# Performance work log

Measured on AMD Instinct MI355X. Metric: run time of the kernel, lower is better.

## Reference

```python
import jax, jax.numpy as jnp
import numpy as np

C_IN = 256
C_OUT = 256
NUM_HEADS = 4
C_HEAD = C_OUT // NUM_HEADS  # 64
ALPHA = 0.2
NEG_FILL = -9e15


def setup_inputs() -> dict:
    key = jax.random.key(0)
    k1, k2, k3, k4, k5 = jax.random.split(key, 5)
    B, N = 1, 4096
    node_feats = jax.random.normal(k1, (B, N, C_IN), dtype=jnp.float32)
    adj_matrix = jax.random.randint(k2, (B, N, N), 0, 2, dtype=jnp.int32)
    # xavier_uniform with gain=1.414 on projection weight (fan_in=C_IN, fan_out=C_OUT)
    lim_w = 1.414 * np.sqrt(6.0 / (C_IN + C_OUT))
    W = jax.random.uniform(k3, (C_IN, C_OUT), dtype=jnp.float32, minval=-lim_w, maxval=lim_w)
    b = jnp.zeros((C_OUT,), dtype=jnp.float32)
    lim_a = 1.414 * np.sqrt(6.0 / (NUM_HEADS + 2 * C_HEAD))
    a = jax.random.uniform(k4, (NUM_HEADS, 2 * C_HEAD), dtype=jnp.float32, minval=-lim_a, maxval=lim_a)
    return {"node_feats": node_feats, "adj_matrix": adj_matrix, "W": W, "b": b, "a": a}


def reference(node_feats, adj_matrix, W, b, a):
    B, N, _ = node_feats.shape
    # linear projection -> (B, N, H, C_HEAD)
    feats = (node_feats @ W + b).reshape(B, N, NUM_HEADS, C_HEAD)
    # attention logit for edge (i -> j): a_src . h_i + a_dst . h_j, per head
    a_src, a_dst = a[:, :C_HEAD], a[:, C_HEAD:]
    src = jnp.einsum('bnhc,hc->bnh', feats, a_src)  # indexed by row i
    dst = jnp.einsum('bnhc,hc->bnh', feats, a_dst)  # indexed by col j
    logits = src[:, :, None, :] + dst[:, None, :, :]  # (B, N, N, H)
    logits = jnp.where(logits >= 0, logits, ALPHA * logits)  # LeakyReLU(0.2)
    attn = jnp.where(adj_matrix[..., None] == 1, logits, NEG_FILL)
    probs = jax.nn.softmax(attn, axis=2)  # softmax over source nodes j
    out = jnp.einsum('bijh,bjhc->bihc', probs, feats)
    return out.reshape(B, N, NUM_HEADS * C_HEAD)  # concat heads
```

## Files before the change

kernel.cpp:

```cpp
#include <hip/hip_runtime.h>

#define NN 4096
#define C 256
#define NH 4
#define CH 64
#define JSPLIT 16
#define JSLICE (NN / JSPLIT)
#define NJT (JSLICE / 32)

typedef float f32x4 __attribute__((ext_vector_type(4)));
typedef __bf16 b16x8 __attribute__((ext_vector_type(8)));
typedef unsigned short u16x8 __attribute__((ext_vector_type(8)));
typedef unsigned int u32x4 __attribute__((ext_vector_type(4)));

__device__ inline float fast_exp2(float x) {
#if __has_builtin(__builtin_amdgcn_exp2f)
  return __builtin_amdgcn_exp2f(x);
#else
  return exp2f(x);
#endif
}

__device__ inline unsigned pack2bf(float f0, float f1) {
  unsigned u0 = __float_as_uint(f0) + 0x8000u;
  unsigned u1 = __float_as_uint(f1) + 0x8000u;
  return __builtin_amdgcn_perm(u1, u0, 0x07060302u);
}

__global__ __launch_bounds__(256) void k_prep(
    const int* __restrict__ adj, const float* __restrict__ X,
    const float* __restrict__ W, unsigned char* __restrict__ packed,
    unsigned short* __restrict__ Xbf, unsigned short* __restrict__ WT) {
  const int b = blockIdx.x, t = threadIdx.x;
  if (b < 8192) {
    const int idx = b * 256 + t;
    const int4 a0 = *(const int4*)(adj + (size_t)idx * 8);
    const int4 a1 = *(const int4*)(adj + (size_t)idx * 8 + 4);
    unsigned m = 0;
    m |= (a0.x != 0) ? 1u : 0u;   m |= (a0.y != 0) ? 2u : 0u;
    m |= (a0.z != 0) ? 4u : 0u;   m |= (a0.w != 0) ? 8u : 0u;
    m |= (a1.x != 0) ? 16u : 0u;  m |= (a1.y != 0) ? 32u : 0u;
    m |= (a1.z != 0) ? 64u : 0u;  m |= (a1.w != 0) ? 128u : 0u;
    packed[idx] = (unsigned char)m;
  } else if (b < 9216) {
    const int idx = (b - 8192) * 256 + t;
    const float4 v = ((const float4*)X)[idx];
    uint2 st;
    st.x = pack2bf(v.x, v.y);
    st.y = pack2bf(v.z, v.w);
    ((uint2*)Xbf)[idx] = st;
  } else {
    const int c = b - 9216;
    const float w = W[(size_t)t * C + c];
    WT[(size_t)c * C + t] = (unsigned short)((__float_as_uint(w) + 0x8000u) >> 16);
  }
}

__global__ __launch_bounds__(256) void k_feats(
    const unsigned short* __restrict__ Xbf, const unsigned short* __restrict__ WT,
    const float* __restrict__ bias, const float* __restrict__ av,
    unsigned short* __restrict__ F, float2* __restrict__ srcAB,
    float2* __restrict__ EdT2) {
  const int i0 = blockIdx.x * 16;
  const int h = threadIdx.x >> 6;
  const int lane = threadIdx.x & 63;
  const int q = lane >> 4, n = lane & 15;
  const int c0 = h * CH;
  const float LOG2E = 1.4426950408889634f;

  const f32x4 zero = {0.f, 0.f, 0.f, 0.f};
  f32x4 acc[4];
#pragma unroll
  for (int g = 0; g < 4; ++g) acc[g] = zero;

  const unsigned short* ap = Xbf + (size_t)(i0 + n) * C + q * 8;
#pragma unroll
  for (int kt = 0; kt < 8; ++kt) {
    const b16x8 aF = __builtin_bit_cast(b16x8, *(const u16x8*)(ap + kt * 32));
#pragma unroll
    for (int g = 0; g < 4; ++g) {
      const b16x8 bF = __builtin_bit_cast(b16x8,
          *(const u16x8*)(WT + (size_t)(c0 + g * 16 + n) * C + kt * 32 + q * 8));
      acc[g] = __builtin_amdgcn_mfma_f32_16x16x32_bf16(aF, bF, acc[g], 0, 0, 0);
    }
  }

  float fb[4][4], asv[4], adv[4];
#pragma unroll
  for (int g = 0; g < 4; ++g) {
    const float bs = bias[c0 + g * 16 + n];
    asv[g] = av[h * 128 + g * 16 + n];
    adv[g] = av[h * 128 + 64 + g * 16 + n];
#pragma unroll
    for (int r = 0; r < 4; ++r) fb[g][r] = acc[g][r] + bs;
  }
  const int jt = i0 >> 5, half = (i0 >> 4) & 1;
  const int qp = half * 2 + (q >> 1);
#pragma unroll
  for (int g = 0; g < 4; ++g) {
    uint2 st;
    st.x = pack2bf(fb[g][0], fb[g][1]);
    st.y = pack2bf(fb[g][2], fb[g][3]);
    *(uint2*)(F + ((size_t)((jt * NH + h) * 4 + g)) * 512 + (qp * 16 + n) * 8 + 4 * (q & 1)) = st;
  }
#pragma unroll
  for (int r = 0; r < 4; ++r) {
    float p = 0.f, d = 0.f;
#pragma unroll
    for (int g = 0; g < 4; ++g) {
      p = fmaf(fb[g][r], asv[g], p);
      d = fmaf(fb[g][r], adv[g], d);
    }
#pragma unroll
    for (int m = 1; m < 16; m <<= 1) {
      p += __shfl_xor(p, m);
      d += __shfl_xor(d, m);
    }
    if (n == 0) {
      const int row = i0 + q * 4 + r;
      const float dL = d * LOG2E;
      EdT2[(size_t)h * NN + row] = make_float2(fast_exp2(dL), fast_exp2(0.2f * dL));
      const float x = p + 16.0f;
      const float m2 = fmaxf(x, 0.2f * x) * LOG2E;
      srcAB[(size_t)row * NH + h] = make_float2(
          fast_exp2(fmaf(p, LOG2E, -m2)),
          fast_exp2(fmaf(0.2f * p, LOG2E, -m2)));
    }
  }
}

__global__ __launch_bounds__(256, 4) void k_attn(
    const unsigned char* __restrict__ packed,
    const unsigned short* __restrict__ F,
    const float2* __restrict__ srcAB, const float2* __restrict__ EdT2,
    _Float16* __restrict__ pacc, float* __restrict__ lpart) {
  const int slice = blockIdx.x;
  const int i0 = blockIdx.y * 32;
  const int h = threadIdx.x >> 6;
  const int lane = threadIdx.x & 63;
  const int q = lane >> 4, n = lane & 15;
  const int jbase = slice * JSLICE;

  const int r0 = i0 + n, r1 = i0 + 16 + n;
  const float2 ab0 = srcAB[(size_t)r0 * NH + h];
  const float2 ab1 = srcAB[(size_t)r1 * NH + h];

  const f32x4 zero = {0.f, 0.f, 0.f, 0.f};
  f32x4 acc0[4], acc1[4], lacc0 = zero, lacc1 = zero;
#pragma unroll
  for (int g = 0; g < 4; ++g) { acc0[g] = zero; acc1[g] = zero; }

  u16x8 ou;
#pragma unroll
  for (int jj = 0; jj < 8; ++jj) ou[jj] = 0x3F80;
  const b16x8 ones = __builtin_bit_cast(b16x8, ou);

  const uint2 m20 = *(const uint2*)(packed + (size_t)r0 * 512 + (jbase >> 3) + q * 8);
  const uint2 m21 = *(const uint2*)(packed + (size_t)r1 * 512 + (jbase >> 3) + q * 8);

  const float* dp2 = (const float*)(EdT2 + (size_t)h * NN + jbase);
  const unsigned short* fp = F + ((size_t)((jbase >> 5) * NH + h) * 4) * 512 + lane * 8;

#pragma unroll
  for (int a = 0; a < 4; ++a) {
#pragma unroll
    for (int b = 0; b < 2; ++b) {
      const int jt = a * 2 + b;
      b16x8 bF[4];
#pragma unroll
      for (int g = 0; g < 4; ++g)
        bF[g] = __builtin_bit_cast(b16x8,
            *(const u16x8*)(fp + (size_t)(jt * NH * 4 + g) * 512));

      const int w0 = b ? (int)m20.y : (int)m20.x;
      const int w1 = b ? (int)m21.y : (int)m21.x;
      const unsigned Mb0 = (unsigned(__shfl(w0, a * 16 + n)) >> (q * 8)) & 0xffu;
      const unsigned Mb1 = (unsigned(__shfl(w1, a * 16 + n)) >> (q * 8)) & 0xffu;

      const float* dq = dp2 + jt * 64 + q * 16;
      const float4 dd0 = *(const float4*)(dq);
      const float4 dd1 = *(const float4*)(dq + 4);
      const float4 dd2 = *(const float4*)(dq + 8);
      const float4 dd3 = *(const float4*)(dq + 12);
      const float4 dd[4] = {dd0, dd1, dd2, dd3};

      u32x4 pk0, pk1;
#pragma unroll
      for (int k = 0; k < 4; ++k) {
        const float4 d = dd[k];
        const float e00 = (Mb0 & (1u << (2 * k))) ? fmaxf(d.x * ab0.x, d.y * ab0.y) : 0.f;
        const float e01 = (Mb0 & (2u << (2 * k))) ? fmaxf(d.z * ab0.x, d.w * ab0.y) : 0.f;
        const float e10 = (Mb1 & (1u << (2 * k))) ? fmaxf(d.x * ab1.x, d.y * ab1.y) : 0.f;
        const float e11 = (Mb1 & (2u << (2 * k))) ? fmaxf(d.z * ab1.x, d.w * ab1.y) : 0.f;
        pk0[k] = pack2bf(e00, e01);
        pk1[k] = pack2bf(e10, e11);
      }
      const b16x8 E0 = __builtin_bit_cast(b16x8, pk0);
      const b16x8 E1 = __builtin_bit_cast(b16x8, pk1);
#pragma unroll
      for (int g = 0; g < 4; ++g) {
        acc0[g] = __builtin_amdgcn_mfma_f32_16x16x32_bf16(E0, bF[g], acc0[g], 0, 0, 0);
        acc1[g] = __builtin_amdgcn_mfma_f32_16x16x32_bf16(E1, bF[g], acc1[g], 0, 0, 0);
      }
      lacc0 = __builtin_amdgcn_mfma_f32_16x16x32_bf16(E0, ones, lacc0, 0, 0, 0);
      lacc1 = __builtin_amdgcn_mfma_f32_16x16x32_bf16(E1, ones, lacc1, 0, 0, 0);
    }
  }

#pragma unroll
  for (int g = 0; g < 4; ++g)
#pragma unroll
    for (int r = 0; r < 4; ++r) {
      const int col = h * CH + g * 16 + n;
      pacc[((size_t)slice * NN + i0 + q * 4 + r) * C + col] = (_Float16)acc0[g][r];
      pacc[((size_t)slice * NN + i0 + 16 + q * 4 + r) * C + col] = (_Float16)acc1[g][r];
    }
  if (n == 0) {
#pragma unroll
    for (int r = 0; r < 4; ++r) {
      lpart[((size_t)slice * NN + i0 + q * 4 + r) * NH + h] = lacc0[r];
      lpart[((size_t)slice * NN + i0 + 16 + q * 4 + r) * NH + h] = lacc1[r];
    }
  }
}

__global__ __launch_bounds__(256) void k_final(
    const _Float16* __restrict__ pacc, const float* __restrict__ lpart,
    float* __restrict__ out) {
  const int i = blockIdx.x;
  const int c = threadIdx.x;
  const int h = c >> 6;
  float l = 0.f, sa = 0.f;
#pragma unroll
  for (int sp = 0; sp < JSPLIT; ++sp) {
    l += lpart[((size_t)sp * NN + i) * NH + h];
    sa += (float)pacc[((size_t)sp * NN + i) * C + c];
  }
  out[(size_t)i * C + c] = sa / l;
}

extern "C" void kernel_launch(void* const* d_in, const int* in_sizes, int n_in,
                              void* d_out, int out_size, void* d_ws, size_t ws_size,
                              hipStream_t stream) {
  const float* nf   = (const float*)d_in[0];
  const int* adj    = (const int*)d_in[1];
  const float* W    = (const float*)d_in[2];
  const float* bias = (const float*)d_in[3];
  const float* av   = (const float*)d_in[4];
  float* out = (float*)d_out;

  char* ws = (char*)d_ws;
  unsigned char* packed  = (unsigned char*)ws;
  unsigned short* Xbf    = (unsigned short*)(ws + (2u << 20));
  unsigned short* WT     = (unsigned short*)(ws + (4u << 20));
  unsigned short* F      = (unsigned short*)(ws + (4u << 20) + (256u << 10));
  float2* srcAB = (float2*)(ws + (6u << 20) + (256u << 10));
  float2* EdT2  = (float2*)(ws + (6u << 20) + (384u << 10));
  float* lpart  = (float*)(ws + (6u << 20) + (512u << 10));
  _Float16* pacc = (_Float16*)(ws + (8u << 20));

  k_prep<<<9472, 256, 0, stream>>>(adj, nf, W, packed, Xbf, WT);
  k_feats<<<NN / 16, 256, 0, stream>>>(Xbf, WT, bias, av, F, srcAB, EdT2);
  dim3 g2(JSPLIT, NN / 32);
  k_attn<<<g2, 256, 0, stream>>>(packed, F, srcAB, EdT2, pacc, lpart);
  k_final<<<NN, 256, 0, stream>>>(pacc, lpart, out);
}
```

Measured before the change: 145.7 us.

## Move adjacency packing into feats kernel, remap attn blocks, vectorize final reduce

```diff
diff --git a/kernel.cpp b/kernel.cpp
--- a/kernel.cpp
+++ b/kernel.cpp
@@ -12,6 +12,7 @@
 typedef __bf16 b16x8 __attribute__((ext_vector_type(8)));
 typedef unsigned short u16x8 __attribute__((ext_vector_type(8)));
 typedef unsigned int u32x4 __attribute__((ext_vector_type(4)));
+typedef _Float16 f16x2 __attribute__((ext_vector_type(2)));
 
 __device__ inline float fast_exp2(float x) {
 #if __has_builtin(__builtin_amdgcn_exp2f)
@@ -28,12 +29,31 @@
 }
 
 __global__ __launch_bounds__(256) void k_prep(
-    const int* __restrict__ adj, const float* __restrict__ X,
-    const float* __restrict__ W, unsigned char* __restrict__ packed,
+    const float* __restrict__ X, const float* __restrict__ W,
     unsigned short* __restrict__ Xbf, unsigned short* __restrict__ WT) {
   const int b = blockIdx.x, t = threadIdx.x;
-  if (b < 8192) {
+  if (b < 1024) {
     const int idx = b * 256 + t;
+    const float4 v = ((const float4*)X)[idx];
+    uint2 st;
+    st.x = pack2bf(v.x, v.y);
+    st.y = pack2bf(v.z, v.w);
+    ((uint2*)Xbf)[idx] = st;
+  } else {
+    const int c = b - 1024;
+    const float w = W[(size_t)t * C + c];
+    WT[(size_t)c * C + t] = (unsigned short)((__float_as_uint(w) + 0x8000u) >> 16);
+  }
+}
+
+__global__ __launch_bounds__(256) void k_feats(
+    const unsigned short* __restrict__ Xbf, const unsigned short* __restrict__ WT,
+    const float* __restrict__ bias, const float* __restrict__ av,
+    const int* __restrict__ adj, unsigned char* __restrict__ packed,
+    unsigned short* __restrict__ F, float2* __restrict__ srcAB,
+    float2* __restrict__ EdT2) {
+  if (blockIdx.x >= 256) {
+    const int idx = (blockIdx.x - 256) * 256 + threadIdx.x;
     const int4 a0 = *(const int4*)(adj + (size_t)idx * 8);
     const int4 a1 = *(const int4*)(adj + (size_t)idx * 8 + 4);
     unsigned m = 0;
@@ -42,25 +62,8 @@
     m |= (a1.x != 0) ? 16u : 0u;  m |= (a1.y != 0) ? 32u : 0u;
     m |= (a1.z != 0) ? 64u : 0u;  m |= (a1.w != 0) ? 128u : 0u;
     packed[idx] = (unsigned char)m;
-  } else if (b < 9216) {
-    const int idx = (b - 8192) * 256 + t;
-    const float4 v = ((const float4*)X)[idx];
-    uint2 st;
-    st.x = pack2bf(v.x, v.y);
-    st.y = pack2bf(v.z, v.w);
-    ((uint2*)Xbf)[idx] = st;
-  } else {
-    const int c = b - 9216;
-    const float w = W[(size_t)t * C + c];
-    WT[(size_t)c * C + t] = (unsigned short)((__float_as_uint(w) + 0x8000u) >> 16);
-  }
-}
-
-__global__ __launch_bounds__(256) void k_feats(
-    const unsigned short* __restrict__ Xbf, const unsigned short* __restrict__ WT,
-    const float* __restrict__ bias, const float* __restrict__ av,
-    unsigned short* __restrict__ F, float2* __restrict__ srcAB,
-    float2* __restrict__ EdT2) {
+    return;
+  }
   const int i0 = blockIdx.x * 16;
   const int h = threadIdx.x >> 6;
   const int lane = threadIdx.x & 63;
@@ -129,13 +132,14 @@
   }
 }
 
-__global__ __launch_bounds__(256, 4) void k_attn(
+__global__ __launch_bounds__(256, 8) void k_attn(
     const unsigned char* __restrict__ packed,
     const unsigned short* __restrict__ F,
     const float2* __restrict__ srcAB, const float2* __restrict__ EdT2,
     _Float16* __restrict__ pacc, float* __restrict__ lpart) {
-  const int slice = blockIdx.x;
-  const int i0 = blockIdx.y * 32;
+  const int wgid = blockIdx.x;
+  const int slice = (wgid & 7) + (((wgid >> 10) & 1) << 3);
+  const int i0 = ((wgid >> 3) & 127) * 32;
   const int h = threadIdx.x >> 6;
   const int lane = threadIdx.x & 63;
   const int q = lane >> 4, n = lane & 15;
@@ -227,16 +231,21 @@
 __global__ __launch_bounds__(256) void k_final(
     const _Float16* __restrict__ pacc, const float* __restrict__ lpart,
     float* __restrict__ out) {
-  const int i = blockIdx.x;
-  const int c = threadIdx.x;
-  const int h = c >> 6;
-  float l = 0.f, sa = 0.f;
+  const int t = threadIdx.x;
+  const int row = blockIdx.x * 2 + (t >> 7);
+  const int tc = t & 127;
+  const int c2 = tc * 2;
+  const int h = tc >> 5;
+  float l = 0.f, sa0 = 0.f, sa1 = 0.f;
 #pragma unroll
   for (int sp = 0; sp < JSPLIT; ++sp) {
-    l += lpart[((size_t)sp * NN + i) * NH + h];
-    sa += (float)pacc[((size_t)sp * NN + i) * C + c];
-  }
-  out[(size_t)i * C + c] = sa / l;
+    l += lpart[((size_t)sp * NN + row) * NH + h];
+    const f16x2 v = *(const f16x2*)(pacc + ((size_t)sp * NN + row) * C + c2);
+    sa0 += (float)v[0];
+    sa1 += (float)v[1];
+  }
+  const float rl = 1.0f / l;
+  *(float2*)(out + (size_t)row * C + c2) = make_float2(sa0 * rl, sa1 * rl);
 }
 
 extern "C" void kernel_launch(void* const* d_in, const int* in_sizes, int n_in,
@@ -259,9 +268,8 @@
   float* lpart  = (float*)(ws + (6u << 20) + (512u << 10));
   _Float16* pacc = (_Float16*)(ws + (8u << 20));
 
-  k_prep<<<9472, 256, 0, stream>>>(adj, nf, W, packed, Xbf, WT);
-  k_feats<<<NN / 16, 256, 0, stream>>>(Xbf, WT, bias, av, F, srcAB, EdT2);
-  dim3 g2(JSPLIT, NN / 32);
-  k_attn<<<g2, 256, 0, stream>>>(packed, F, srcAB, EdT2, pacc, lpart);
-  k_final<<<NN, 256, 0, stream>>>(pacc, lpart, out);
-}
+  k_prep<<<1280, 256, 0, stream>>>(nf, W, Xbf, WT);
+  k_feats<<<8448, 256, 0, stream>>>(Xbf, WT, bias, av, adj, packed, F, srcAB, EdT2);
+  k_attn<<<2048, 256, 0, stream>>>(packed, F, srcAB, EdT2, pacc, lpart);
+  k_final<<<NN / 2, 256, 0, stream>>>(pacc, lpart, out);
+}
```

Result: slower. 287.4 us (+97.3%).
